# Optimization experiments

Hardware: AMD Instinct MI355X
Metric: run time of the kernel (lower is better)

The kernel has to match this reference:

```python
import jax, jax.numpy as jnp
import numpy as np
from jax import lax

THETA = 0.7
DN = ('NCHW', 'OIHW', 'NCHW')


def setup_inputs() -> dict:
    key = jax.random.key(0)
    k1, k2 = jax.random.split(key)
    x = jax.random.normal(k1, (16, 64, 128, 128), dtype=jnp.float32)
    W = jax.random.normal(k2, (64, 64, 3, 3), dtype=jnp.float32) * 0.05
    return {"x": x, "W": W}


def _shift_sum(x):
    # Sum of the center view plus the 8 shifted views of the reflection-padded
    # input (the original code's lt/mt/rt/lm/center/mr/ld/md/rd slices cover
    # exactly the full 3x3 neighborhood of the padded tensor).
    B, C, H, W_ = x.shape
    xp = jnp.pad(x, ((0, 0), (0, 0), (1, 1), (1, 1)), mode='reflect')
    s = jnp.zeros_like(x)
    for dy in range(3):
        for dx in range(3):
            s = s + xp[:, :, dy:dy + H, dx:dx + W_]
    return s


def reference(x, W):
    # Conv is linear and bias=False, so sum_i conv(shift_i(x)) == conv(sum_i shift_i(x)).
    s = _shift_sum(x)  # [B,C,H,W]
    out_normal = lax.conv_general_dilated(s, W, (1, 1), [(1, 1), (1, 1)], dimension_numbers=DN)
    kernel_diff = W.sum(axis=(2, 3))[:, :, None, None]  # [C_out,C_in,1,1]
    out_diff = lax.conv_general_dilated(s, kernel_diff, (1, 1), [(0, 0), (0, 0)], dimension_numbers=DN)
    return out_normal - THETA * out_diff
```

## Files before the change

kernel.cpp:

```cpp
#include <hip/hip_runtime.h>
#include <stdint.h>


#define THETA 0.7f

typedef __attribute__((ext_vector_type(8))) short bf16x8;
typedef __attribute__((ext_vector_type(16))) float f32x16;

__device__ inline unsigned short f2bf(float f) {
    unsigned u = __float_as_uint(f);
    u = (u + 0x7FFFu + ((u >> 16) & 1u)) >> 16;
    return (unsigned short)u;
}
__device__ inline void async16(const void* g, void* l) {
    __builtin_amdgcn_global_load_lds(
        (const __attribute__((address_space(1))) unsigned int*)g,
        (__attribute__((address_space(3))) unsigned int*)l, 16, 0, 0);
}

__global__ void weff_kernel(const float* __restrict__ W, unsigned short* __restrict__ Wt2) {
    int t = blockIdx.x * blockDim.x + threadIdx.x;
    if (t >= 512) return;
    int o = t >> 3;
    int ch8 = t & 7;
    int c0 = ch8 * 8;
    int ic = ch8 >> 1;
    int mf = o >> 5;
    int lane = (o & 31) | ((ch8 & 1) << 5);

    float v[8][9];
    float tsum[8];
#pragma unroll
    for (int j = 0; j < 8; j++) {
        const float* w = W + ((size_t)o * 64 + c0 + j) * 9;
        float sum = 0.f;
#pragma unroll
        for (int k = 0; k < 9; k++) { v[j][k] = w[k]; sum += v[j][k]; }
        tsum[j] = sum;
    }
#pragma unroll
    for (int tap = 0; tap < 9; tap++) {
        unsigned short* dst = Wt2 + (((size_t)(tap * 4 + ic) * 2 + mf) * 64 + lane) * 8;
#pragma unroll
        for (int j = 0; j < 8; j++) {
            float val = v[j][tap] - ((tap == 4) ? THETA * tsum[j] : 0.f);
            dst[j] = f2bf(val);
        }
    }
}

__global__ __launch_bounds__(512) void boxsumT_kernel(const float* __restrict__ x,
                                                      unsigned short* __restrict__ s) {
    __shared__ unsigned short tb[128 * 72];
    int bid = blockIdx.x;
    int b = bid >> 4;
    int h0 = (bid & 15) * 8;
    int tid = threadIdx.x;
    int w4 = tid & 31;
    int cg = tid >> 5;
    int c0 = cg * 4;
    const float* xp = x + ((size_t)(b * 64 + c0)) * 16384 + w4 * 4;

    float4 A[4], B[4], C[4];
    int hm = (h0 == 0) ? 1 : h0 - 1;
#pragma unroll
    for (int cc = 0; cc < 4; cc++) {
        A[cc] = *(const float4*)(xp + (size_t)cc * 16384 + hm * 128);
        B[cc] = *(const float4*)(xp + (size_t)cc * 16384 + h0 * 128);
        C[cc] = *(const float4*)(xp + (size_t)cc * 16384 + (h0 + 1) * 128);
    }

#pragma unroll
    for (int r = 0; r < 8; r++) {
        float4 Cn[4];
        if (r < 7) {
            int hn = h0 + 2 + r;
            if (hn > 127) hn = 126;
#pragma unroll
            for (int cc = 0; cc < 4; cc++)
                Cn[cc] = *(const float4*)(xp + (size_t)cc * 16384 + hn * 128);
        }

        unsigned short res[4][4];
#pragma unroll
        for (int cc = 0; cc < 4; cc++) {
            float4 vs;
            vs.x = A[cc].x + B[cc].x + C[cc].x;
            vs.y = A[cc].y + B[cc].y + C[cc].y;
            vs.z = A[cc].z + B[cc].z + C[cc].z;
            vs.w = A[cc].w + B[cc].w + C[cc].w;
            float L = __shfl_up(vs.w, 1, 32);
            float R = __shfl_down(vs.x, 1, 32);
            float sx = (w4 == 0) ? vs.x + 2.f * vs.y : L + vs.x + vs.y;
            float sy = vs.x + vs.y + vs.z;
            float sz = vs.y + vs.z + vs.w;
            float sw = (w4 == 31) ? 2.f * vs.z + vs.w : vs.z + vs.w + R;
            res[cc][0] = f2bf(sx);
            res[cc][1] = f2bf(sy);
            res[cc][2] = f2bf(sz);
            res[cc][3] = f2bf(sw);
        }
#pragma unroll
        for (int k = 0; k < 4; k++) {
            ushort4 o4 = make_ushort4(res[0][k], res[1][k], res[2][k], res[3][k]);
            *(ushort4*)(tb + (size_t)(w4 * 4 + k) * 72 + c0) = o4;
        }
#pragma unroll
        for (int cc = 0; cc < 4; cc++) { A[cc] = B[cc]; B[cc] = C[cc]; C[cc] = Cn[cc]; }
        __syncthreads();

        unsigned short* sp = s + (((size_t)b * 128 + (h0 + r)) * 128) * 64;
#pragma unroll
        for (int f = 0; f < 2; f++) {
            int id = f * 512 + tid;
            int w = id >> 3, c8 = id & 7;
            bf16x8 v = *(const bf16x8*)(tb + (size_t)w * 72 + c8 * 8);
            *(bf16x8*)(sp + (size_t)w * 64 + c8 * 8) = v;
        }
        __syncthreads();
    }
}

__global__ __launch_bounds__(256, 2) void conv_kernel(const unsigned short* __restrict__ s,
                                                      const unsigned short* __restrict__ Wt2,
                                                      float* __restrict__ out) {
    __shared__ __align__(16) unsigned short sS[6 * 66 * 64];

    int bid = blockIdx.x;
    int b = bid >> 6;
    int h0 = ((bid >> 1) & 31) * 4;
    int w0 = (bid & 1) * 64;
    int tid = threadIdx.x;
    int lane = tid & 63;
    int wv = tid >> 6;
    int n32 = lane & 31;
    int q2 = lane >> 5;

    const char* sb = (const char*)s + ((size_t)b * 128) * 16384;

    int4 z = make_int4(0, 0, 0, 0);
    if (h0 == 0)
        for (int i = tid; i < 528; i += 256) *(int4*)((char*)sS + (size_t)i * 16) = z;
    if (h0 == 124)
        for (int i = tid; i < 528; i += 256) *(int4*)((char*)sS + (size_t)(5 * 528 + i) * 16) = z;

    if (tid < 96) {
        int r = tid >> 4;
        int side = (tid >> 3) & 1;
        int g = tid & 7;
        int slot = side ? 65 : 0;
        int hg = h0 - 1 + r;
        int wg = w0 - 1 + slot;
        int4 v = z;
        if ((unsigned)hg < 128u && (unsigned)wg < 128u) {
            int u = g ^ (slot & 7);
            v = *(const int4*)(sb + (size_t)hg * 16384 + (size_t)wg * 128 + u * 16);
        }
        *(int4*)((char*)sS + (size_t)(r * 528 + slot * 8 + g) * 16) = v;
    }

#pragma unroll
    for (int it = 0; it < 12; it++) {
        int row = it >> 1;
        int hg = h0 - 1 + row;
        if (hg < 0 || hg > 127) continue;
        int rem = (it & 1) * 256 + tid;
        int slot = 1 + (rem >> 3);
        int g = rem & 7;
        int wg = w0 + (rem >> 3);
        int u = g ^ (slot & 7);
        async16(sb + (size_t)hg * 16384 + (size_t)wg * 128 + u * 16,
                (char*)sS + (size_t)(row * 528 + 8 + rem) * 16);
    }
    __syncthreads();

    int p0[3][4];
#pragma unroll
    for (int kx = 0; kx < 3; kx++)
#pragma unroll
        for (int ic = 0; ic < 4; ic++) {
            int slot = n32 + kx;
            int g = (ic * 2 + q2) ^ (slot & 7);
            p0[kx][ic] = slot * 64 + g * 8;
        }

    f32x16 acc[2][2];
#pragma unroll
    for (int mf = 0; mf < 2; mf++)
#pragma unroll
        for (int nf = 0; nf < 2; nf++)
#pragma unroll
            for (int r = 0; r < 16; r++) acc[mf][nf][r] = 0.f;

    bf16x8 Af[8], An[8];
#pragma unroll
    for (int ic = 0; ic < 4; ic++)
#pragma unroll
        for (int mf = 0; mf < 2; mf++)
            Af[ic * 2 + mf] = *(const bf16x8*)(Wt2 + (((size_t)(0 * 4 + ic) * 2 + mf) * 64 + lane) * 8);

#pragma unroll
    for (int tap = 0; tap < 9; tap++) {
        int ky = tap / 3, kx = tap % 3;
        if (tap < 8) {
#pragma unroll
            for (int ic = 0; ic < 4; ic++)
#pragma unroll
                for (int mf = 0; mf < 2; mf++)
                    An[ic * 2 + mf] = *(const bf16x8*)(Wt2 + (((size_t)((tap + 1) * 4 + ic) * 2 + mf) * 64 + lane) * 8);
        }
#pragma unroll
        for (int ic = 0; ic < 4; ic++) {
            const unsigned short* bp = sS + (size_t)(wv + ky) * 4224 + p0[kx][ic];
            bf16x8 b0 = *(const bf16x8*)(bp);
            bf16x8 b1 = *(const bf16x8*)(bp + 2048);
            acc[0][0] = __builtin_amdgcn_mfma_f32_32x32x16_bf16(Af[ic * 2 + 0], b0, acc[0][0], 0, 0, 0);
            acc[0][1] = __builtin_amdgcn_mfma_f32_32x32x16_bf16(Af[ic * 2 + 0], b1, acc[0][1], 0, 0, 0);
            acc[1][0] = __builtin_amdgcn_mfma_f32_32x32x16_bf16(Af[ic * 2 + 1], b0, acc[1][0], 0, 0, 0);
            acc[1][1] = __builtin_amdgcn_mfma_f32_32x32x16_bf16(Af[ic * 2 + 1], b1, acc[1][1], 0, 0, 0);
        }
        if (tap < 8) {
#pragma unroll
            for (int k = 0; k < 8; k++) Af[k] = An[k];
        }
    }

    float* ob = out + ((size_t)b * 64) * 16384 + (size_t)(h0 + wv) * 128 + w0;
#pragma unroll
    for (int mf = 0; mf < 2; mf++)
#pragma unroll
        for (int nf = 0; nf < 2; nf++)
#pragma unroll
            for (int r = 0; r < 16; r++) {
                int o = mf * 32 + (r & 3) + 8 * (r >> 2) + 4 * q2;
                ob[(size_t)o * 16384 + nf * 32 + n32] = acc[mf][nf][r];
            }
}

extern "C" void kernel_launch(void* const* d_in, const int* in_sizes, int n_in,
                              void* d_out, int out_size, void* d_ws, size_t ws_size,
                              hipStream_t stream) {
    const float* x = (const float*)d_in[0];
    const float* W = (const float*)d_in[1];
    float* outp = (float*)d_out;

    unsigned short* Wt2 = (unsigned short*)d_ws;
    unsigned short* s = (unsigned short*)((char*)d_ws + 73728);

    weff_kernel<<<2, 256, 0, stream>>>(W, Wt2);
    boxsumT_kernel<<<256, 512, 0, stream>>>(x, s);
    conv_kernel<<<1024, 256, 0, stream>>>(s, Wt2, outp);
}
```

Before: 142.2 us.

## Give each conv wave two output rows and restructure box-sum tiling

The conv kernel now runs 128 threads, and each wave computes two output rows. Each weight fragment is reused across twice as many MFMAs, with the A fragments double-buffered. The box-sum kernel now covers 8 channels per thread over 4 rows per block and double-buffers the LDS transpose tile, so it synchronises once per two rows. The weight index arithmetic is simplified without changing the layout. The exchange is higher register pressure (64 accumulator floats plus two A buffers) and fewer waves per block, which could hurt occupancy and latency hiding.

```diff
diff --git a/kernel.cpp b/kernel.cpp
--- a/kernel.cpp
+++ b/kernel.cpp
@@ -40,7 +40,7 @@
     }
 #pragma unroll
     for (int tap = 0; tap < 9; tap++) {
-        unsigned short* dst = Wt2 + (((size_t)(tap * 4 + ic) * 2 + mf) * 64 + lane) * 8;
+        unsigned short* dst = Wt2 + (size_t)(tap * 8 + ic * 2 + mf) * 512 + (size_t)lane * 8;
 #pragma unroll
         for (int j = 0; j < 8; j++) {
             float val = v[j][tap] - ((tap == 4) ? THETA * tsum[j] : 0.f);
@@ -49,46 +49,46 @@
     }
 }
 
-__global__ __launch_bounds__(512) void boxsumT_kernel(const float* __restrict__ x,
+__global__ __launch_bounds__(256) void boxsumT_kernel(const float* __restrict__ x,
                                                       unsigned short* __restrict__ s) {
-    __shared__ unsigned short tb[128 * 72];
+    __shared__ unsigned short tb[2][128 * 68];
     int bid = blockIdx.x;
-    int b = bid >> 4;
-    int h0 = (bid & 15) * 8;
+    int b = bid >> 5;
+    int h0 = (bid & 31) * 4;
     int tid = threadIdx.x;
     int w4 = tid & 31;
     int cg = tid >> 5;
-    int c0 = cg * 4;
+    int c0 = cg * 8;
     const float* xp = x + ((size_t)(b * 64 + c0)) * 16384 + w4 * 4;
 
-    float4 A[4], B[4], C[4];
+    float4 A[8], Bv[8], C[8];
     int hm = (h0 == 0) ? 1 : h0 - 1;
 #pragma unroll
-    for (int cc = 0; cc < 4; cc++) {
-        A[cc] = *(const float4*)(xp + (size_t)cc * 16384 + hm * 128);
-        B[cc] = *(const float4*)(xp + (size_t)cc * 16384 + h0 * 128);
-        C[cc] = *(const float4*)(xp + (size_t)cc * 16384 + (h0 + 1) * 128);
-    }
-
-#pragma unroll
-    for (int r = 0; r < 8; r++) {
-        float4 Cn[4];
-        if (r < 7) {
+    for (int cc = 0; cc < 8; cc++) {
+        A[cc]  = *(const float4*)(xp + (size_t)cc * 16384 + hm * 128);
+        Bv[cc] = *(const float4*)(xp + (size_t)cc * 16384 + h0 * 128);
+        C[cc]  = *(const float4*)(xp + (size_t)cc * 16384 + (h0 + 1) * 128);
+    }
+
+#pragma unroll
+    for (int r = 0; r < 4; r++) {
+        float4 Cn[8];
+        if (r < 3) {
             int hn = h0 + 2 + r;
             if (hn > 127) hn = 126;
 #pragma unroll
-            for (int cc = 0; cc < 4; cc++)
+            for (int cc = 0; cc < 8; cc++)
                 Cn[cc] = *(const float4*)(xp + (size_t)cc * 16384 + hn * 128);
         }
 
-        unsigned short res[4][4];
-#pragma unroll
-        for (int cc = 0; cc < 4; cc++) {
+        unsigned short res[8][4];
+#pragma unroll
+        for (int cc = 0; cc < 8; cc++) {
             float4 vs;
-            vs.x = A[cc].x + B[cc].x + C[cc].x;
-            vs.y = A[cc].y + B[cc].y + C[cc].y;
-            vs.z = A[cc].z + B[cc].z + C[cc].z;
-            vs.w = A[cc].w + B[cc].w + C[cc].w;
+            vs.x = A[cc].x + Bv[cc].x + C[cc].x;
+            vs.y = A[cc].y + Bv[cc].y + C[cc].y;
+            vs.z = A[cc].z + Bv[cc].z + C[cc].z;
+            vs.w = A[cc].w + Bv[cc].w + C[cc].w;
             float L = __shfl_up(vs.w, 1, 32);
             float R = __shfl_down(vs.x, 1, 32);
             float sx = (w4 == 0) ? vs.x + 2.f * vs.y : L + vs.x + vs.y;
@@ -100,28 +100,36 @@
             res[cc][2] = f2bf(sz);
             res[cc][3] = f2bf(sw);
         }
+        unsigned short* trow = tb[r & 1];
 #pragma unroll
         for (int k = 0; k < 4; k++) {
-            ushort4 o4 = make_ushort4(res[0][k], res[1][k], res[2][k], res[3][k]);
-            *(ushort4*)(tb + (size_t)(w4 * 4 + k) * 72 + c0) = o4;
-        }
-#pragma unroll
-        for (int cc = 0; cc < 4; cc++) { A[cc] = B[cc]; B[cc] = C[cc]; C[cc] = Cn[cc]; }
-        __syncthreads();
-
-        unsigned short* sp = s + (((size_t)b * 128 + (h0 + r)) * 128) * 64;
-#pragma unroll
-        for (int f = 0; f < 2; f++) {
-            int id = f * 512 + tid;
-            int w = id >> 3, c8 = id & 7;
-            bf16x8 v = *(const bf16x8*)(tb + (size_t)w * 72 + c8 * 8);
-            *(bf16x8*)(sp + (size_t)w * 64 + c8 * 8) = v;
-        }
-        __syncthreads();
-    }
-}
-
-__global__ __launch_bounds__(256, 2) void conv_kernel(const unsigned short* __restrict__ s,
+            ushort4 lo = make_ushort4(res[0][k], res[1][k], res[2][k], res[3][k]);
+            ushort4 hi = make_ushort4(res[4][k], res[5][k], res[6][k], res[7][k]);
+            *(ushort4*)(trow + (size_t)(w4 * 4 + k) * 68 + c0) = lo;
+            *(ushort4*)(trow + (size_t)(w4 * 4 + k) * 68 + c0 + 4) = hi;
+        }
+#pragma unroll
+        for (int cc = 0; cc < 8; cc++) { A[cc] = Bv[cc]; Bv[cc] = C[cc]; C[cc] = Cn[cc]; }
+
+        if (r & 1) {
+            __syncthreads();
+            unsigned short* sp = s + (((size_t)b * 128 + (h0 + r - 1)) * 128) * 64;
+#pragma unroll
+            for (int f = 0; f < 16; f++) {
+                int id = f * 256 + tid;
+                int rr = id >> 11;
+                int rem = id & 2047;
+                int w = rem >> 4;
+                int c4 = (rem & 15) * 4;
+                ushort4 v = *(const ushort4*)(tb[rr] + (size_t)w * 68 + c4);
+                *(ushort4*)(sp + (size_t)rr * 8192 + (size_t)w * 64 + c4) = v;
+            }
+            __syncthreads();
+        }
+    }
+}
+
+__global__ __launch_bounds__(128, 2) void conv_kernel(const unsigned short* __restrict__ s,
                                                       const unsigned short* __restrict__ Wt2,
                                                       float* __restrict__ out) {
     __shared__ __align__(16) unsigned short sS[6 * 66 * 64];
@@ -140,9 +148,9 @@
 
     int4 z = make_int4(0, 0, 0, 0);
     if (h0 == 0)
-        for (int i = tid; i < 528; i += 256) *(int4*)((char*)sS + (size_t)i * 16) = z;
+        for (int i = tid; i < 528; i += 128) *(int4*)((char*)sS + (size_t)i * 16) = z;
     if (h0 == 124)
-        for (int i = tid; i < 528; i += 256) *(int4*)((char*)sS + (size_t)(5 * 528 + i) * 16) = z;
+        for (int i = tid; i < 528; i += 128) *(int4*)((char*)sS + (size_t)(5 * 528 + i) * 16) = z;
 
     if (tid < 96) {
         int r = tid >> 4;
@@ -160,11 +168,11 @@
     }
 
 #pragma unroll
-    for (int it = 0; it < 12; it++) {
-        int row = it >> 1;
+    for (int it = 0; it < 24; it++) {
+        int row = it >> 2;
         int hg = h0 - 1 + row;
         if (hg < 0 || hg > 127) continue;
-        int rem = (it & 1) * 256 + tid;
+        int rem = (it & 3) * 128 + tid;
         int slot = 1 + (rem >> 3);
         int g = rem & 7;
         int wg = w0 + (rem >> 3);
@@ -184,57 +192,63 @@
             p0[kx][ic] = slot * 64 + g * 8;
         }
 
-    f32x16 acc[2][2];
+    f32x16 acc[2][2][2];
 #pragma unroll
     for (int mf = 0; mf < 2; mf++)
 #pragma unroll
-        for (int nf = 0; nf < 2; nf++)
-#pragma unroll
-            for (int r = 0; r < 16; r++) acc[mf][nf][r] = 0.f;
-
-    bf16x8 Af[8], An[8];
-#pragma unroll
-    for (int ic = 0; ic < 4; ic++)
-#pragma unroll
-        for (int mf = 0; mf < 2; mf++)
-            Af[ic * 2 + mf] = *(const bf16x8*)(Wt2 + (((size_t)(0 * 4 + ic) * 2 + mf) * 64 + lane) * 8);
+        for (int r = 0; r < 2; r++)
+#pragma unroll
+            for (int nf = 0; nf < 2; nf++)
+#pragma unroll
+                for (int e = 0; e < 16; e++) acc[mf][r][nf][e] = 0.f;
+
+    const unsigned short* wbase = Wt2 + (size_t)lane * 8;
+    bf16x8 Af[2][8];
+#pragma unroll
+    for (int k = 0; k < 8; k++)
+        Af[0][k] = *(const bf16x8*)(wbase + (size_t)k * 512);
 
 #pragma unroll
     for (int tap = 0; tap < 9; tap++) {
+        int cur = tap & 1;
+        if (tap < 8) {
+#pragma unroll
+            for (int k = 0; k < 8; k++)
+                Af[cur ^ 1][k] = *(const bf16x8*)(wbase + (size_t)((tap + 1) * 8 + k) * 512);
+        }
         int ky = tap / 3, kx = tap % 3;
-        if (tap < 8) {
-#pragma unroll
-            for (int ic = 0; ic < 4; ic++)
-#pragma unroll
-                for (int mf = 0; mf < 2; mf++)
-                    An[ic * 2 + mf] = *(const bf16x8*)(Wt2 + (((size_t)((tap + 1) * 4 + ic) * 2 + mf) * 64 + lane) * 8);
-        }
 #pragma unroll
         for (int ic = 0; ic < 4; ic++) {
-            const unsigned short* bp = sS + (size_t)(wv + ky) * 4224 + p0[kx][ic];
-            bf16x8 b0 = *(const bf16x8*)(bp);
-            bf16x8 b1 = *(const bf16x8*)(bp + 2048);
-            acc[0][0] = __builtin_amdgcn_mfma_f32_32x32x16_bf16(Af[ic * 2 + 0], b0, acc[0][0], 0, 0, 0);
-            acc[0][1] = __builtin_amdgcn_mfma_f32_32x32x16_bf16(Af[ic * 2 + 0], b1, acc[0][1], 0, 0, 0);
-            acc[1][0] = __builtin_amdgcn_mfma_f32_32x32x16_bf16(Af[ic * 2 + 1], b0, acc[1][0], 0, 0, 0);
-            acc[1][1] = __builtin_amdgcn_mfma_f32_32x32x16_bf16(Af[ic * 2 + 1], b1, acc[1][1], 0, 0, 0);
-        }
-        if (tap < 8) {
-#pragma unroll
-            for (int k = 0; k < 8; k++) Af[k] = An[k];
-        }
-    }
-
-    float* ob = out + ((size_t)b * 64) * 16384 + (size_t)(h0 + wv) * 128 + w0;
+            const unsigned short* bp = sS + (size_t)(wv * 2 + ky) * 4224 + p0[kx][ic];
+            bf16x8 b00 = *(const bf16x8*)(bp);
+            bf16x8 b01 = *(const bf16x8*)(bp + 2048);
+            bf16x8 b10 = *(const bf16x8*)(bp + 4224);
+            bf16x8 b11 = *(const bf16x8*)(bp + 4224 + 2048);
+            bf16x8 a0 = Af[cur][ic * 2 + 0];
+            bf16x8 a1 = Af[cur][ic * 2 + 1];
+            acc[0][0][0] = __builtin_amdgcn_mfma_f32_32x32x16_bf16(a0, b00, acc[0][0][0], 0, 0, 0);
+            acc[0][0][1] = __builtin_amdgcn_mfma_f32_32x32x16_bf16(a0, b01, acc[0][0][1], 0, 0, 0);
+            acc[0][1][0] = __builtin_amdgcn_mfma_f32_32x32x16_bf16(a0, b10, acc[0][1][0], 0, 0, 0);
+            acc[0][1][1] = __builtin_amdgcn_mfma_f32_32x32x16_bf16(a0, b11, acc[0][1][1], 0, 0, 0);
+            acc[1][0][0] = __builtin_amdgcn_mfma_f32_32x32x16_bf16(a1, b00, acc[1][0][0], 0, 0, 0);
+            acc[1][0][1] = __builtin_amdgcn_mfma_f32_32x32x16_bf16(a1, b01, acc[1][0][1], 0, 0, 0);
+            acc[1][1][0] = __builtin_amdgcn_mfma_f32_32x32x16_bf16(a1, b10, acc[1][1][0], 0, 0, 0);
+            acc[1][1][1] = __builtin_amdgcn_mfma_f32_32x32x16_bf16(a1, b11, acc[1][1][1], 0, 0, 0);
+        }
+    }
+
+    float* ob = out + ((size_t)b * 64) * 16384 + (size_t)(h0 + wv * 2) * 128 + w0;
 #pragma unroll
     for (int mf = 0; mf < 2; mf++)
 #pragma unroll
-        for (int nf = 0; nf < 2; nf++)
-#pragma unroll
-            for (int r = 0; r < 16; r++) {
-                int o = mf * 32 + (r & 3) + 8 * (r >> 2) + 4 * q2;
-                ob[(size_t)o * 16384 + nf * 32 + n32] = acc[mf][nf][r];
-            }
+        for (int r = 0; r < 2; r++)
+#pragma unroll
+            for (int nf = 0; nf < 2; nf++)
+#pragma unroll
+                for (int e = 0; e < 16; e++) {
+                    int o = mf * 32 + (e & 3) + 8 * (e >> 2) + 4 * q2;
+                    ob[(size_t)o * 16384 + (size_t)r * 128 + nf * 32 + n32] = acc[mf][r][nf][e];
+                }
 }
 
 extern "C" void kernel_launch(void* const* d_in, const int* in_sizes, int n_in,
@@ -248,6 +262,6 @@
     unsigned short* s = (unsigned short*)((char*)d_ws + 73728);
 
     weff_kernel<<<2, 256, 0, stream>>>(W, Wt2);
-    boxsumT_kernel<<<256, 512, 0, stream>>>(x, s);
-    conv_kernel<<<1024, 256, 0, stream>>>(s, Wt2, outp);
-}
+    boxsumT_kernel<<<512, 256, 0, stream>>>(x, s);
+    conv_kernel<<<1024, 128, 0, stream>>>(s, Wt2, outp);
+}
```

Result: slower. 171.9 us (+20.9%).
